# Performance work log

Hardware: AMD Instinct MI355X
Metric: run time of the kernel (lower is better)

Reference implementation:

```python
import jax, jax.numpy as jnp
import numpy as np

EPS_LN = 1e-5
NEG_SLOPE = 0.2
NUM_GRAPHS = 64


def layer_norm(h, g, b):
    mu = h.mean(-1, keepdims=True)
    var = ((h - mu) ** 2).mean(-1, keepdims=True)
    return (h - mu) * jax.lax.rsqrt(var + EPS_LN) * g + b


def segment_softmax(alpha, dst, n):
    # alpha: [E2, H], softmax over edges sharing the same dst node
    m = jax.ops.segment_max(alpha, dst, num_segments=n)
    m = jnp.where(jnp.isfinite(m), m, 0.0)
    e = jnp.exp(alpha - m[dst])
    s = jax.ops.segment_sum(e, dst, num_segments=n)
    return e / (s[dst] + 1e-16)


def gat_conv(h, src, dst, eattr, W, We, a_s, a_d, a_e, bias, H, C):
    # PyG GATConv: shared src/dst linear, edge features, self-loops (fill='mean')
    N = h.shape[0]
    x = (h @ W).reshape(N, H, C)  # [N,H,C]
    loop = jnp.arange(N)
    src2 = jnp.concatenate([src, loop])
    dst2 = jnp.concatenate([dst, loop])
    loop_attr = jnp.broadcast_to(eattr.mean(0, keepdims=True), (N, eattr.shape[1]))
    e2 = jnp.concatenate([eattr, loop_attr], 0)
    eh = (e2 @ We).reshape(-1, H, C)  # [E2,H,C]
    alpha = (x * a_s).sum(-1)[src2] + (x * a_d).sum(-1)[dst2] + (eh * a_e).sum(-1)
    alpha = jax.nn.leaky_relu(alpha, NEG_SLOPE)  # [E2,H]
    alpha = segment_softmax(alpha, dst2, N)
    out = jax.ops.segment_sum(x[src2] * alpha[:, :, None], dst2, num_segments=N)
    return out.reshape(N, H * C) + bias


def setup_inputs():
    key = jax.random.key(0)
    ks = jax.random.split(key, 24)
    N, E = 50000, 400000
    Fin, Hd, H, ed = 6, 64, 4, 1
    d0 = Hd * H          # 256 after layer0
    C1 = 128 // H        # 32, layer1 per-head out
    s = 0.1
    inp = {
        'x': jax.random.normal(ks[0], (N, Fin), jnp.float32),
        'edge_index': jax.random.randint(ks[1], (2, E), 0, N),
        'edge_attr': jax.random.uniform(ks[2], (E, ed), jnp.float32),
        'batch': jnp.sort(jax.random.randint(ks[3], (N,), 0, NUM_GRAPHS)),
        'W_in': jax.random.normal(ks[4], (Fin, Hd), jnp.float32) * s,
        'b_in': jnp.zeros((Hd,), jnp.float32),
        'l0_W': jax.random.normal(ks[5], (Hd, H * Hd), jnp.float32) * s,
        'l0_We': jax.random.normal(ks[6], (ed, H * Hd), jnp.float32) * s,
        'l0_as': jax.random.normal(ks[7], (H, Hd), jnp.float32) * s,
        'l0_ad': jax.random.normal(ks[8], (H, Hd), jnp.float32) * s,
        'l0_ae': jax.random.normal(ks[9], (H, Hd), jnp.float32) * s,
        'l0_b': jnp.zeros((H * Hd,), jnp.float32),
        'ln0_g': jnp.ones((d0,), jnp.float32),
        'ln0_b': jnp.zeros((d0,), jnp.float32),
        'l1_W': jax.random.normal(ks[10], (d0, H * C1), jnp.float32) * s,
        'l1_We': jax.random.normal(ks[11], (ed, H * C1), jnp.float32) * s,
        'l1_as': jax.random.normal(ks[12], (H, C1), jnp.float32) * s,
        'l1_ad': jax.random.normal(ks[13], (H, C1), jnp.float32) * s,
        'l1_ae': jax.random.normal(ks[14], (H, C1), jnp.float32) * s,
        'l1_b': jnp.zeros((H * C1,), jnp.float32),
        'ln1_g': jnp.ones((128,), jnp.float32),
        'ln1_b': jnp.zeros((128,), jnp.float32),
    }
    return inp


def reference(x, edge_index, edge_attr, batch, W_in, b_in,
              l0_W, l0_We, l0_as, l0_ad, l0_ae, l0_b, ln0_g, ln0_b,
              l1_W, l1_We, l1_as, l1_ad, l1_ae, l1_b, ln1_g, ln1_b):
    src, dst = edge_index[0], edge_index[1]
    H = 4
    h = x @ W_in + b_in                                  # input_proj
    h = gat_conv(h, src, dst, edge_attr, l0_W, l0_We, l0_as, l0_ad, l0_ae, l0_b, H, 64)
    h = layer_norm(h, ln0_g, ln0_b)
    h = jax.nn.elu(h)                                    # dropout off (eval)
    h = gat_conv(h, src, dst, edge_attr, l1_W, l1_We, l1_as, l1_ad, l1_ae, l1_b, H, 32)
    h = layer_norm(h, ln1_g, ln1_b)
    cnt = jax.ops.segment_sum(jnp.ones((h.shape[0],), h.dtype), batch, num_segments=NUM_GRAPHS)
    h_mean = jax.ops.segment_sum(h, batch, num_segments=NUM_GRAPHS) / jnp.maximum(cnt, 1.0)[:, None]
    h_max = jax.ops.segment_max(h, batch, num_segments=NUM_GRAPHS)
    return (h_mean + h_max) / 2.0
```

## Files before the change

kernel.cpp:

```cpp
#include <hip/hip_runtime.h>
#include <math.h>

#define EPS_LN   1e-5f
#define NEG_SLOPE 0.2f
#define NUM_GRAPHS 64
#define POOL_SPLIT 16

__device__ __forceinline__ float red64(float v) {
    #pragma unroll
    for (int m = 32; m > 0; m >>= 1) v += __shfl_xor(v, m);
    return v;
}
__device__ __forceinline__ float red32(float v) {
    #pragma unroll
    for (int m = 16; m > 0; m >>= 1) v += __shfl_xor(v, m);
    return v;
}

__global__ __launch_bounds__(256) void k_input_proj(
    const float* __restrict__ x, const float* __restrict__ Win,
    const float* __restrict__ bin, float* __restrict__ h, int N)
{
    int t = blockIdx.x * 256 + threadIdx.x;
    if (t >= N * 64) return;
    int n = t >> 6, c = t & 63;
    float acc = bin[c];
    const float* xr = x + n * 6;
    #pragma unroll
    for (int k = 0; k < 6; ++k) acc += xr[k] * Win[k * 64 + c];
    h[t] = acc;
}

__global__ __launch_bounds__(256) void k_prep(
    const float* __restrict__ We0, const float* __restrict__ ae0,
    const float* __restrict__ We1, const float* __restrict__ ae1,
    float* __restrict__ wedot0, float* __restrict__ wedot1)
{
    __shared__ float red[256];
    int t = threadIdx.x;
    red[t] = We0[t] * ae0[t];
    __syncthreads();
    for (int s = 32; s > 0; s >>= 1) { if ((t & 63) < s) red[t] += red[t + s]; __syncthreads(); }
    if ((t & 63) == 0) wedot0[t >> 6] = red[t];
    __syncthreads();
    red[t] = (t < 128) ? We1[t] * ae1[t] : 0.f;
    __syncthreads();
    for (int s = 16; s > 0; s >>= 1) { if (t < 128 && (t & 31) < s) red[t] += red[t + s]; __syncthreads(); }
    if (t < 128 && (t & 31) == 0) wedot1[t >> 5] = red[t];
}

__global__ __launch_bounds__(256) void k_esum_partial(const float* __restrict__ ea, float* __restrict__ part, int E)
{
    __shared__ float red[256];
    int t = threadIdx.x;
    float s = 0.f;
    for (int i = blockIdx.x * 256 + t; i < E; i += gridDim.x * 256) s += ea[i];
    red[t] = s; __syncthreads();
    for (int k = 128; k > 0; k >>= 1) { if (t < k) red[t] += red[t + k]; __syncthreads(); }
    if (t == 0) part[blockIdx.x] = red[0];
}
__global__ __launch_bounds__(256) void k_esum_final(const float* __restrict__ part, int B, float* __restrict__ mean_out, int E)
{
    __shared__ float red[256];
    int t = threadIdx.x;
    red[t] = (t < B) ? part[t] : 0.f; __syncthreads();
    for (int k = 128; k > 0; k >>= 1) { if (t < k) red[t] += red[t + k]; __syncthreads(); }
    if (t == 0) *mean_out = red[0] / (float)E;
}

__global__ __launch_bounds__(256) void k_counts_init(int* __restrict__ counts, int N)
{
    int t = blockIdx.x * 256 + threadIdx.x;
    if (t < N) counts[t] = 1;
}
__global__ __launch_bounds__(256) void k_count(const int* __restrict__ dst, int* __restrict__ counts, int E)
{
    int e = blockIdx.x * 256 + threadIdx.x;
    if (e < E) atomicAdd(&counts[dst[e]], 1);
}
__global__ __launch_bounds__(256) void k_scan_partial(const int* __restrict__ counts, int* __restrict__ bsum, int N)
{
    __shared__ int red[256];
    int b = blockIdx.x, t = threadIdx.x;
    int base = b * 1024 + t * 4;
    int s = 0;
    #pragma unroll
    for (int i = 0; i < 4; ++i) { int idx = base + i; if (idx < N) s += counts[idx]; }
    red[t] = s; __syncthreads();
    for (int k = 128; k > 0; k >>= 1) { if (t < k) red[t] += red[t + k]; __syncthreads(); }
    if (t == 0) bsum[b] = red[0];
}
__global__ __launch_bounds__(64) void k_scan_bsums(const int* __restrict__ bsum, int* __restrict__ bpre, int B)
{
    __shared__ int s[64];
    int t = threadIdx.x;
    int v = (t < B) ? bsum[t] : 0;
    s[t] = v; __syncthreads();
    for (int off = 1; off < 64; off <<= 1) {
        int u = (t >= off) ? s[t - off] : 0; __syncthreads();
        s[t] += u; __syncthreads();
    }
    if (t < B) bpre[t] = s[t] - v;
}
__global__ __launch_bounds__(256) void k_scan_chunk(
    const int* __restrict__ counts, const int* __restrict__ bpre,
    int* __restrict__ row_ptr, int N, int E2)
{
    __shared__ int s[256];
    int b = blockIdx.x, t = threadIdx.x;
    int base = b * 1024 + t * 4;
    int l0 = (base + 0 < N) ? counts[base + 0] : 0;
    int l1 = (base + 1 < N) ? counts[base + 1] : 0;
    int l2 = (base + 2 < N) ? counts[base + 2] : 0;
    int l3 = (base + 3 < N) ? counts[base + 3] : 0;
    int lsum = l0 + l1 + l2 + l3;
    s[t] = lsum; __syncthreads();
    for (int off = 1; off < 256; off <<= 1) {
        int u = (t >= off) ? s[t - off] : 0; __syncthreads();
        s[t] += u; __syncthreads();
    }
    int run = bpre[b] + s[t] - lsum;
    if (base + 0 < N) row_ptr[base + 0] = run; run += l0;
    if (base + 1 < N) row_ptr[base + 1] = run; run += l1;
    if (base + 2 < N) row_ptr[base + 2] = run; run += l2;
    if (base + 3 < N) row_ptr[base + 3] = run;
    if (b == 0 && t == 0) row_ptr[N] = E2;
}
__global__ __launch_bounds__(256) void k_cursor_init(const int* __restrict__ row_ptr, int* __restrict__ cursor, int N)
{
    int t = blockIdx.x * 256 + threadIdx.x;
    if (t < N) cursor[t] = row_ptr[t];
}
__global__ __launch_bounds__(256) void k_place(
    const int* __restrict__ dst, int* __restrict__ cursor, int* __restrict__ eids, int E, int N)
{
    int e = blockIdx.x * 256 + threadIdx.x;
    if (e >= E + N) return;
    int d = (e < E) ? dst[e] : (e - E);
    int pos = atomicAdd(&cursor[d], 1);
    eids[pos] = e;
}
__global__ __launch_bounds__(256) void k_rowsort(const int* __restrict__ row_ptr, int* __restrict__ eids, int N)
{
    int n = blockIdx.x * 256 + threadIdx.x;
    if (n >= N) return;
    int r0 = row_ptr[n], r1 = row_ptr[n + 1];
    for (int i = r0 + 1; i < r1; ++i) {
        int key = eids[i];
        int j = i - 1;
        while (j >= r0 && eids[j] > key) { eids[j + 1] = eids[j]; --j; }
        eids[j + 1] = key;
    }
}

#define G0_NPW 4
__global__ __launch_bounds__(256) void k_gemm0(
    const float* __restrict__ h, const float* __restrict__ W0, float* __restrict__ x0, int N)
{
    __shared__ float Wl[64 * 256];
    int t = threadIdx.x;
    for (int i = t; i < 64 * 256; i += 256) Wl[i] = W0[i];
    __syncthreads();
    int wave = t >> 6, lane = t & 63;
    int gw = blockIdx.x * 4 + wave;
    int stride = gridDim.x * 4 * G0_NPW;
    for (int nb = gw * G0_NPW; nb < N; nb += stride) {
        float hv[G0_NPW];
        float acc[G0_NPW][4] = {};
        #pragma unroll
        for (int p = 0; p < G0_NPW; ++p) {
            int n = nb + p;
            hv[p] = (n < N) ? h[(size_t)n * 64 + lane] : 0.f;
        }
        for (int k = 0; k < 64; ++k) {
            float w0 = Wl[k * 256 + lane];
            float w1 = Wl[k * 256 + lane + 64];
            float w2 = Wl[k * 256 + lane + 128];
            float w3 = Wl[k * 256 + lane + 192];
            #pragma unroll
            for (int p = 0; p < G0_NPW; ++p) {
                float hk = __shfl(hv[p], k);
                acc[p][0] += hk * w0; acc[p][1] += hk * w1;
                acc[p][2] += hk * w2; acc[p][3] += hk * w3;
            }
        }
        #pragma unroll
        for (int p = 0; p < G0_NPW; ++p) {
            int n = nb + p;
            if (n < N) {
                float* o = x0 + (size_t)n * 256;
                o[lane] = acc[p][0]; o[lane + 64] = acc[p][1];
                o[lane + 128] = acc[p][2]; o[lane + 192] = acc[p][3];
            }
        }
    }
}

__global__ __launch_bounds__(256) void k_gemm1(
    const float* __restrict__ h0, const float* __restrict__ W1,
    float* __restrict__ x1, int N)
{
    __shared__ float Wq[256 * 32];
    __shared__ float Ht[64 * 128];
    const int q = blockIdx.y;
    const int nb = blockIdx.x * 128;
    int t = threadIdx.x;
    for (int i = t; i < 256 * 32; i += 256)
        Wq[i] = W1[(i >> 5) * 128 + q * 32 + (i & 31)];
    const int tc = t & 7, tr = t >> 3;
    const int r0 = tr * 4, c0 = tc * 4;
    const int kg = t & 15, rbase = t >> 4;
    float acc[4][4] = {};
    #pragma unroll
    for (int kc = 0; kc < 4; ++kc) {
        __syncthreads();
        #pragma unroll
        for (int j = 0; j < 8; ++j) {
            int row = j * 16 + rbase;
            int n = nb + row;
            float4 v = make_float4(0.f, 0.f, 0.f, 0.f);
            if (n < N)
                v = *reinterpret_cast<const float4*>(h0 + (size_t)n * 256 + kc * 64 + kg * 4);
            #pragma unroll
            for (int i = 0; i < 4; ++i) {
                int k = kg * 4 + i;
                float e = (i == 0) ? v.x : (i == 1) ? v.y : (i == 2) ? v.z : v.w;
                Ht[k * 128 + (row ^ (((k >> 2) & 7) << 2))] = e;
            }
        }
        __syncthreads();
        #pragma unroll 8
        for (int k2 = 0; k2 < 64; ++k2) {
            float4 hh = *reinterpret_cast<const float4*>(
                &Ht[k2 * 128 + (r0 ^ (((k2 >> 2) & 7) << 2))]);
            float4 ww = *reinterpret_cast<const float4*>(&Wq[(kc * 64 + k2) * 32 + c0]);
            acc[0][0] += hh.x * ww.x; acc[0][1] += hh.x * ww.y; acc[0][2] += hh.x * ww.z; acc[0][3] += hh.x * ww.w;
            acc[1][0] += hh.y * ww.x; acc[1][1] += hh.y * ww.y; acc[1][2] += hh.y * ww.z; acc[1][3] += hh.y * ww.w;
            acc[2][0] += hh.z * ww.x; acc[2][1] += hh.z * ww.y; acc[2][2] += hh.z * ww.z; acc[2][3] += hh.z * ww.w;
            acc[3][0] += hh.w * ww.x; acc[3][1] += hh.w * ww.y; acc[3][2] += hh.w * ww.z; acc[3][3] += hh.w * ww.w;
        }
    }
    #pragma unroll
    for (int i = 0; i < 4; ++i) {
        int n = nb + r0 + i;
        if (n < N)
            *reinterpret_cast<float4*>(x1 + (size_t)n * 128 + q * 32 + c0) =
                make_float4(acc[i][0], acc[i][1], acc[i][2], acc[i][3]);
    }
}

template <int HC>
__global__ __launch_bounds__(256) void k_attn(
    const float* __restrict__ x, const float* __restrict__ a_s, const float* __restrict__ a_d,
    float* __restrict__ as_n, float* __restrict__ ad_n, int N)
{
    int n = (blockIdx.x * 256 + threadIdx.x) >> 6;
    int lane = threadIdx.x & 63;
    if (n >= N) return;
    const float* xr = x + (size_t)n * HC;
    #pragma unroll
    for (int j = 0; j < HC / 64; ++j) {
        int ch = j * 64 + lane;
        float v = xr[ch];
        float ps = v * a_s[ch], pd = v * a_d[ch];
        if (HC == 256) {
            ps = red64(ps); pd = red64(pd);
            if (lane == 0) { as_n[n * 4 + j] = ps; ad_n[n * 4 + j] = pd; }
        } else {
            ps = red32(ps); pd = red32(pd);
            if ((lane & 31) == 0) {
                int hh = 2 * j + (lane >> 5);
                as_n[n * 4 + hh] = ps; ad_n[n * 4 + hh] = pd;
            }
        }
    }
}

template <bool WRITE_SRC>
__global__ __launch_bounds__(256) void k_edgeprep(
    const int* __restrict__ row_ptr, const int* __restrict__ eids,
    const int* __restrict__ src, const float* __restrict__ eattr,
    const float* __restrict__ emean_p, const float* __restrict__ wedot,
    const float* __restrict__ as_n, const float* __restrict__ ad_n,
    int* __restrict__ srcp, float4* __restrict__ alpha, int N, int E)
{
    int n = (blockIdx.x * 256 + threadIdx.x) >> 6;
    int lane = threadIdx.x & 63;
    if (n >= N) return;
    float emean = *emean_p;
    float wd0 = wedot[0], wd1 = wedot[1], wd2 = wedot[2], wd3 = wedot[3];
    float adv0 = ad_n[n * 4 + 0], adv1 = ad_n[n * 4 + 1];
    float adv2 = ad_n[n * 4 + 2], adv3 = ad_n[n * 4 + 3];
    int r0 = row_ptr[n], r1 = row_ptr[n + 1];
    for (int i = r0 + lane; i < r1; i += 64) {
        int eid = eids[i];
        int sn; float ev;
        if (eid < E) { sn = src[eid]; ev = eattr[eid]; } else { sn = n; ev = emean; }
        if (WRITE_SRC) srcp[i] = sn;
        const float* as4 = as_n + (size_t)sn * 4;
        float a0 = as4[0] + adv0 + ev * wd0;
        float a1 = as4[1] + adv1 + ev * wd1;
        float a2 = as4[2] + adv2 + ev * wd2;
        float a3 = as4[3] + adv3 + ev * wd3;
        a0 = (a0 > 0.f) ? a0 : NEG_SLOPE * a0;
        a1 = (a1 > 0.f) ? a1 : NEG_SLOPE * a1;
        a2 = (a2 > 0.f) ? a2 : NEG_SLOPE * a2;
        a3 = (a3 > 0.f) ? a3 : NEG_SLOPE * a3;
        alpha[i] = make_float4(a0, a1, a2, a3);
    }
}

template <int HC, int VEC, bool DO_ELU>
__global__ __launch_bounds__(256) void k_agg(
    const float* __restrict__ x, const int* __restrict__ row_ptr,
    const int* __restrict__ srcp, const float* __restrict__ alpha,
    const float* __restrict__ bias, const float* __restrict__ lng, const float* __restrict__ lnb,
    float* __restrict__ out, int N)
{
    int n = (blockIdx.x * 256 + threadIdx.x) >> 6;
    int lane = threadIdx.x & 63;
    if (n >= N) return;
    int hh = lane >> 4;
    int r0 = row_ptr[n], r1 = row_ptr[n + 1];

    float m = -INFINITY, s = 0.f;
    float acc[VEC] = {};
    for (int i = r0; i < r1; ++i) {
        int sn = srcp[i];
        float a = alpha[(size_t)i * 4 + hh];
        float nm = fmaxf(m, a);
        float sc = __expf(m - nm);
        float w  = __expf(a - nm);
        m = nm;
        s = s * sc + w;
        const float* xr = x + (size_t)sn * HC + lane * VEC;
        if constexpr (VEC == 4) {
            float4 xv = *reinterpret_cast<const float4*>(xr);
            acc[0] = acc[0] * sc + w * xv.x;
            acc[1] = acc[1] * sc + w * xv.y;
            acc[2] = acc[2] * sc + w * xv.z;
            acc[3] = acc[3] * sc + w * xv.w;
        } else {
            float2 xv = *reinterpret_cast<const float2*>(xr);
            acc[0] = acc[0] * sc + w * xv.x;
            acc[1] = acc[1] * sc + w * xv.y;
        }
    }
    float inv = 1.f / (s + 1e-16f);

    int ch0 = lane * VEC;
    float v[VEC];
    #pragma unroll
    for (int i = 0; i < VEC; ++i) v[i] = acc[i] * inv + bias[ch0 + i];
    float ls = 0.f;
    #pragma unroll
    for (int i = 0; i < VEC; ++i) ls += v[i];
    ls = red64(ls);
    float mu = ls / (float)HC;
    float lv = 0.f;
    #pragma unroll
    for (int i = 0; i < VEC; ++i) { float d = v[i] - mu; lv += d * d; }
    lv = red64(lv);
    float rs = rsqrtf(lv / (float)HC + EPS_LN);
    float o[VEC];
    #pragma unroll
    for (int i = 0; i < VEC; ++i) {
        float y = (v[i] - mu) * rs * lng[ch0 + i] + lnb[ch0 + i];
        if (DO_ELU) y = (y > 0.f) ? y : (expm1f(y));
        o[i] = y;
    }
    float* orow = out + (size_t)n * HC + ch0;
    if constexpr (VEC == 4) *reinterpret_cast<float4*>(orow) = make_float4(o[0], o[1], o[2], o[3]);
    else                    *reinterpret_cast<float2*>(orow) = make_float2(o[0], o[1]);
}

__global__ __launch_bounds__(128) void k_bounds(const int* __restrict__ batch, int* __restrict__ gstart, int N)
{
    int g = threadIdx.x;
    if (g > NUM_GRAPHS) return;
    int lo = 0, hi = N;
    while (lo < hi) { int mid = (lo + hi) >> 1; if (batch[mid] < g) lo = mid + 1; else hi = mid; }
    gstart[g] = lo;
}
__global__ __launch_bounds__(128) void k_pool1(
    const float* __restrict__ h1, const int* __restrict__ gstart,
    float* __restrict__ psum, float* __restrict__ pmax)
{
    int g = blockIdx.x, sl = blockIdx.y, c = threadIdx.x;
    int s0 = gstart[g], s1 = gstart[g + 1];
    int cnt = s1 - s0;
    int chunk = (cnt + POOL_SPLIT - 1) / POOL_SPLIT;
    int b0 = s0 + sl * chunk;
    int b1 = min(b0 + chunk, s1);
    float sum = 0.f, mx = -INFINITY;
    for (int n = b0; n < b1; ++n) {
        float v = h1[(size_t)n * 128 + c];
        sum += v; mx = fmaxf(mx, v);
    }
    int o = (g * POOL_SPLIT + sl) * 128 + c;
    psum[o] = sum; pmax[o] = mx;
}
__global__ __launch_bounds__(128) void k_pool2(
    const float* __restrict__ psum, const float* __restrict__ pmax,
    const int* __restrict__ gstart, float* __restrict__ out)
{
    int g = blockIdx.x, c = threadIdx.x;
    float sum = 0.f, mx = -INFINITY;
    #pragma unroll
    for (int sl = 0; sl < POOL_SPLIT; ++sl) {
        int o = (g * POOL_SPLIT + sl) * 128 + c;
        sum += psum[o];
        mx = fmaxf(mx, pmax[o]);
    }
    int cnt = gstart[g + 1] - gstart[g];
    float mean = sum / fmaxf((float)cnt, 1.f);
    out[g * 128 + c] = 0.5f * (mean + mx);
}

extern "C" void kernel_launch(void* const* d_in, const int* in_sizes, int n_in,
                              void* d_out, int out_size, void* d_ws, size_t ws_size,
                              hipStream_t stream)
{
    const float* x     = (const float*)d_in[0];
    const int*   ei    = (const int*)d_in[1];
    const float* eattr = (const float*)d_in[2];
    const int*   batch = (const int*)d_in[3];
    const float* Win   = (const float*)d_in[4];
    const float* bin   = (const float*)d_in[5];
    const float* l0W   = (const float*)d_in[6];
    const float* l0We  = (const float*)d_in[7];
    const float* l0as  = (const float*)d_in[8];
    const float* l0ad  = (const float*)d_in[9];
    const float* l0ae  = (const float*)d_in[10];
    const float* l0b   = (const float*)d_in[11];
    const float* ln0g  = (const float*)d_in[12];
    const float* ln0b  = (const float*)d_in[13];
    const float* l1W   = (const float*)d_in[14];
    const float* l1We  = (const float*)d_in[15];
    const float* l1as  = (const float*)d_in[16];
    const float* l1ad  = (const float*)d_in[17];
    const float* l1ae  = (const float*)d_in[18];
    const float* l1b   = (const float*)d_in[19];
    const float* ln1g  = (const float*)d_in[20];
    const float* ln1b  = (const float*)d_in[21];

    const int N = in_sizes[0] / 6;
    const int E = in_sizes[1] / 2;
    const int E2 = E + N;
    const int* srcI = ei;
    const int* dstI = ei + E;

    char* ws = (char*)d_ws;
    size_t off = 0;
    auto alloc = [&](size_t bytes) -> char* {
        char* p = ws + off;
        off += (bytes + 255) & ~(size_t)255;
        return p;
    };

    float* h      = (float*)alloc((size_t)N * 64 * 4);
    float* x0     = (float*)alloc((size_t)N * 256 * 4);
    float* h0     = (float*)alloc((size_t)N * 256 * 4);
    float* as0    = (float*)alloc((size_t)N * 4 * 4);
    float* ad0    = (float*)alloc((size_t)N * 4 * 4);
    float* as1    = (float*)alloc((size_t)N * 4 * 4);
    float* ad1    = (float*)alloc((size_t)N * 4 * 4);
    int*   row_ptr= (int*)alloc((size_t)(N + 1) * 4);
    int*   counts = (int*)alloc((size_t)N * 4);
    int*   cursor = (int*)alloc((size_t)N * 4);
    int*   eids   = (int*)alloc((size_t)E2 * 4);
    int*   srcp   = (int*)alloc((size_t)E2 * 4);
    float4* alphab= (float4*)alloc((size_t)E2 * 16);
    int*   bsum   = (int*)alloc(64 * 4);
    int*   bpre   = (int*)alloc(64 * 4);
    float* epart  = (float*)alloc(256 * 4);
    float* emean  = (float*)alloc(4);
    float* wedot0 = (float*)alloc(16);
    float* wedot1 = (float*)alloc(16);
    int*   gstart = (int*)alloc((NUM_GRAPHS + 1) * 4);
    float* psum   = (float*)alloc((size_t)NUM_GRAPHS * POOL_SPLIT * 128 * 4);
    float* pmax   = (float*)alloc((size_t)NUM_GRAPHS * POOL_SPLIT * 128 * 4);

    float* x1 = x0;
    float* h1 = x0 + (size_t)N * 128;

    const int B = (N + 1023) / 1024;

    k_input_proj<<<(N * 64 + 255) / 256, 256, 0, stream>>>(x, Win, bin, h, N);
    k_prep<<<1, 256, 0, stream>>>(l0We, l0ae, l1We, l1ae, wedot0, wedot1);
    k_esum_partial<<<256, 256, 0, stream>>>(eattr, epart, E);
    k_esum_final<<<1, 256, 0, stream>>>(epart, 256, emean, E);

    k_counts_init<<<(N + 255) / 256, 256, 0, stream>>>(counts, N);
    k_count<<<(E + 255) / 256, 256, 0, stream>>>(dstI, counts, E);
    k_scan_partial<<<B, 256, 0, stream>>>(counts, bsum, N);
    k_scan_bsums<<<1, 64, 0, stream>>>(bsum, bpre, B);
    k_scan_chunk<<<B, 256, 0, stream>>>(counts, bpre, row_ptr, N, E2);
    k_cursor_init<<<(N + 255) / 256, 256, 0, stream>>>(row_ptr, cursor, N);
    k_place<<<(E2 + 255) / 256, 256, 0, stream>>>(dstI, cursor, eids, E, N);
    k_rowsort<<<(N + 255) / 256, 256, 0, stream>>>(row_ptr, eids, N);

    k_gemm0<<<512, 256, 0, stream>>>(h, l0W, x0, N);
    k_attn<256><<<(N + 3) / 4, 256, 0, stream>>>(x0, l0as, l0ad, as0, ad0, N);
    k_edgeprep<true><<<(N + 3) / 4, 256, 0, stream>>>(
        row_ptr, eids, srcI, eattr, emean, wedot0, as0, ad0, srcp, alphab, N, E);
    k_agg<256, 4, true><<<(N + 3) / 4, 256, 0, stream>>>(
        x0, row_ptr, srcp, (const float*)alphab, l0b, ln0g, ln0b, h0, N);

    k_gemm1<<<dim3((N + 127) / 128, 4), 256, 0, stream>>>(h0, l1W, x1, N);
    k_attn<128><<<(N + 3) / 4, 256, 0, stream>>>(x1, l1as, l1ad, as1, ad1, N);
    k_edgeprep<false><<<(N + 3) / 4, 256, 0, stream>>>(
        row_ptr, eids, srcI, eattr, emean, wedot1, as1, ad1, srcp, alphab, N, E);
    k_agg<128, 2, false><<<(N + 3) / 4, 256, 0, stream>>>(
        x1, row_ptr, srcp, (const float*)alphab, l1b, ln1g, ln1b, h1, N);

    k_bounds<<<1, 128, 0, stream>>>(batch, gstart, N);
    k_pool1<<<dim3(NUM_GRAPHS, POOL_SPLIT), 128, 0, stream>>>(h1, gstart, psum, pmax);
    k_pool2<<<NUM_GRAPHS, 128, 0, stream>>>(psum, pmax, gstart, (float*)d_out);
}
```

Measured before the change: 474.7 us.

## Compute full 128-column output tile per block in layer-1 GEMM with 8x8 register tiles

The layer-1 GEMM previously launched four blocks per 128-row tile, one per 32-column quarter, and each re-read the same h0 rows. Now one block computes all 128 output columns, streaming both h0 and W1 in 32-wide k chunks through shared memory, and each thread holds an 8x8 accumulator tile. This removes the fourfold re-read of h0 and raises arithmetic intensity per shared-memory load. In exchange, register pressure is higher and there are four times fewer blocks, which may lower occupancy.

```diff
diff --git a/kernel.cpp b/kernel.cpp
--- a/kernel.cpp
+++ b/kernel.cpp
@@ -200,52 +200,63 @@
     const float* __restrict__ h0, const float* __restrict__ W1,
     float* __restrict__ x1, int N)
 {
-    __shared__ float Wq[256 * 32];
-    __shared__ float Ht[64 * 128];
-    const int q = blockIdx.y;
+    __shared__ float Wc[32 * 128];
+    __shared__ float Ht[32 * 128];
     const int nb = blockIdx.x * 128;
-    int t = threadIdx.x;
-    for (int i = t; i < 256 * 32; i += 256)
-        Wq[i] = W1[(i >> 5) * 128 + q * 32 + (i & 31)];
-    const int tc = t & 7, tr = t >> 3;
+    const int t = threadIdx.x;
+    const int tc = t & 15, tr = t >> 4;
     const int r0 = tr * 4, c0 = tc * 4;
-    const int kg = t & 15, rbase = t >> 4;
-    float acc[4][4] = {};
-    #pragma unroll
-    for (int kc = 0; kc < 4; ++kc) {
+    const int kg = t & 7, rb = t >> 3;
+    float acc[8][8] = {};
+    for (int kc = 0; kc < 8; ++kc) {
         __syncthreads();
         #pragma unroll
-        for (int j = 0; j < 8; ++j) {
-            int row = j * 16 + rbase;
+        for (int j = 0; j < 4; ++j) {
+            int row = rb + j * 32;
             int n = nb + row;
             float4 v = make_float4(0.f, 0.f, 0.f, 0.f);
             if (n < N)
-                v = *reinterpret_cast<const float4*>(h0 + (size_t)n * 256 + kc * 64 + kg * 4);
+                v = *reinterpret_cast<const float4*>(h0 + (size_t)n * 256 + kc * 32 + kg * 4);
             #pragma unroll
             for (int i = 0; i < 4; ++i) {
                 int k = kg * 4 + i;
                 float e = (i == 0) ? v.x : (i == 1) ? v.y : (i == 2) ? v.z : v.w;
-                Ht[k * 128 + (row ^ (((k >> 2) & 7) << 2))] = e;
+                Ht[k * 128 + (row ^ (k & 28))] = e;
             }
         }
+        #pragma unroll
+        for (int it = 0; it < 4; ++it) {
+            int idx = t * 4 + it * 1024;
+            int k2 = idx >> 7, c = idx & 127;
+            *reinterpret_cast<float4*>(&Wc[idx]) =
+                *reinterpret_cast<const float4*>(W1 + (size_t)(kc * 32 + k2) * 128 + c);
+        }
         __syncthreads();
-        #pragma unroll 8
-        for (int k2 = 0; k2 < 64; ++k2) {
-            float4 hh = *reinterpret_cast<const float4*>(
-                &Ht[k2 * 128 + (r0 ^ (((k2 >> 2) & 7) << 2))]);
-            float4 ww = *reinterpret_cast<const float4*>(&Wq[(kc * 64 + k2) * 32 + c0]);
-            acc[0][0] += hh.x * ww.x; acc[0][1] += hh.x * ww.y; acc[0][2] += hh.x * ww.z; acc[0][3] += hh.x * ww.w;
-            acc[1][0] += hh.y * ww.x; acc[1][1] += hh.y * ww.y; acc[1][2] += hh.y * ww.z; acc[1][3] += hh.y * ww.w;
-            acc[2][0] += hh.z * ww.x; acc[2][1] += hh.z * ww.y; acc[2][2] += hh.z * ww.z; acc[2][3] += hh.z * ww.w;
-            acc[3][0] += hh.w * ww.x; acc[3][1] += hh.w * ww.y; acc[3][2] += hh.w * ww.z; acc[3][3] += hh.w * ww.w;
-        }
-    }
-    #pragma unroll
-    for (int i = 0; i < 4; ++i) {
-        int n = nb + r0 + i;
-        if (n < N)
-            *reinterpret_cast<float4*>(x1 + (size_t)n * 128 + q * 32 + c0) =
+        #pragma unroll 4
+        for (int k2 = 0; k2 < 32; ++k2) {
+            int sw = k2 & 28;
+            float4 hlo = *reinterpret_cast<const float4*>(&Ht[k2 * 128 + (r0 ^ sw)]);
+            float4 hhi = *reinterpret_cast<const float4*>(&Ht[k2 * 128 + ((r0 + 64) ^ sw)]);
+            float4 wlo = *reinterpret_cast<const float4*>(&Wc[k2 * 128 + c0]);
+            float4 whi = *reinterpret_cast<const float4*>(&Wc[k2 * 128 + c0 + 64]);
+            float hr[8] = {hlo.x, hlo.y, hlo.z, hlo.w, hhi.x, hhi.y, hhi.z, hhi.w};
+            float wr[8] = {wlo.x, wlo.y, wlo.z, wlo.w, whi.x, whi.y, whi.z, whi.w};
+            #pragma unroll
+            for (int i = 0; i < 8; ++i)
+                #pragma unroll
+                for (int j = 0; j < 8; ++j)
+                    acc[i][j] += hr[i] * wr[j];
+        }
+    }
+    #pragma unroll
+    for (int i = 0; i < 8; ++i) {
+        int n = nb + ((i < 4) ? (r0 + i) : (r0 + 60 + i));
+        if (n < N) {
+            *reinterpret_cast<float4*>(x1 + (size_t)n * 128 + c0) =
                 make_float4(acc[i][0], acc[i][1], acc[i][2], acc[i][3]);
+            *reinterpret_cast<float4*>(x1 + (size_t)n * 128 + c0 + 64) =
+                make_float4(acc[i][4], acc[i][5], acc[i][6], acc[i][7]);
+        }
     }
 }
 
@@ -507,7 +518,7 @@
     k_agg<256, 4, true><<<(N + 3) / 4, 256, 0, stream>>>(
         x0, row_ptr, srcp, (const float*)alphab, l0b, ln0g, ln0b, h0, N);
 
-    k_gemm1<<<dim3((N + 127) / 128, 4), 256, 0, stream>>>(h0, l1W, x1, N);
+    k_gemm1<<<(N + 127) / 128, 256, 0, stream>>>(h0, l1W, x1, N);
     k_attn<128><<<(N + 3) / 4, 256, 0, stream>>>(x1, l1as, l1ad, as1, ad1, N);
     k_edgeprep<false><<<(N + 3) / 4, 256, 0, stream>>>(
         row_ptr, eids, srcI, eattr, emean, wedot1, as1, ad1, srcp, alphab, N, E);
```

Measured after the change: 443.9 us. -6.5%, faster.
